# Optimization experiments

Hardware: AMD Instinct MI355X
Metric: run time of the kernel (lower is better)

## Reference

```python
import jax, jax.numpy as jnp
import numpy as np

NUM_HEADS = 32
NUM_KV_HEADS = 8
HEAD_DIM = 128
PAGE_SIZE = 16
NUM_PAGES = 512
PAGES_PER_SEQ = 256  # 4096 cached tokens
Q_LEN = 1024
SCALE = 0.08838834764831845  # 1/sqrt(HEAD_DIM)


def setup_inputs() -> dict:
    key = jax.random.key(0)
    k1, k2, k3, k4, k5 = jax.random.split(key, 5)
    q = jax.random.normal(k1, (Q_LEN, NUM_HEADS * HEAD_DIM), dtype=jnp.float32)
    k = jax.random.normal(k2, (Q_LEN, NUM_KV_HEADS * HEAD_DIM), dtype=jnp.float32)
    v = jax.random.normal(k3, (Q_LEN, NUM_KV_HEADS * HEAD_DIM), dtype=jnp.float32)
    # paged KV cache: [num_pages, 2 (k/v), num_kv_heads, page_size, head_dim]
    kv_cache = jax.random.normal(
        k4, (NUM_PAGES, 2, NUM_KV_HEADS, PAGE_SIZE, HEAD_DIM), dtype=jnp.float32)
    block_table = jnp.sort(
        jax.random.randint(k5, (PAGES_PER_SEQ,), 0, NUM_PAGES, dtype=jnp.int32))
    return {"q": q, "k": k, "v": v, "kv_cache": kv_cache,
            "block_table": block_table}


def reference(q, k, v, kv_cache, block_table):
    # reshape flat projections into heads
    q = q.reshape(-1, NUM_HEADS, HEAD_DIM)          # [Tq, H, D]
    k = k.reshape(-1, NUM_KV_HEADS, HEAD_DIM)       # [Tq, Hkv, D]
    v = v.reshape(-1, NUM_KV_HEADS, HEAD_DIM)

    # gather paged KV cache into continuous tensors (all pages full)
    pages = kv_cache[block_table]                   # [P, 2, Hkv, ps, D]
    # per-page [Hkv, ps, D] -> [ps, Hkv, D], then concat along token dim
    past = jnp.transpose(pages, (1, 0, 3, 2, 4))    # [2, P, ps, Hkv, D]
    past = past.reshape(2, -1, NUM_KV_HEADS, HEAD_DIM)
    past_k, past_v = past[0], past[1]               # [Tpast, Hkv, D]

    k_full = jnp.concatenate([past_k, k], axis=0)   # [Tkv, Hkv, D]
    v_full = jnp.concatenate([past_v, v], axis=0)

    # GQA: repeat kv heads to match query heads
    heads_per_kv = NUM_HEADS // NUM_KV_HEADS
    k_full = jnp.repeat(k_full, heads_per_kv, axis=1)  # [Tkv, H, D]
    v_full = jnp.repeat(v_full, heads_per_kv, axis=1)

    qh = jnp.transpose(q, (1, 0, 2))                # [H, Tq, D]
    kh = jnp.transpose(k_full, (1, 0, 2))           # [H, Tkv, D]
    vh = jnp.transpose(v_full, (1, 0, 2))

    scores = jnp.einsum('hqd,hkd->hqk', qh, kh) * SCALE  # [H, Tq, Tkv]

    # prefill causal mask exactly as in the source: triu(ones(q_len, kv_len), 1)
    q_len, kv_len = qh.shape[1], kh.shape[1]
    causal = jnp.triu(jnp.ones((q_len, kv_len), dtype=bool), k=1)
    scores = jnp.where(causal[None, :, :], -jnp.inf, scores)

    attn = jax.nn.softmax(scores.astype(jnp.float32), axis=-1).astype(qh.dtype)
    out = jnp.einsum('hqk,hkd->hqd', attn, vh)      # [H, Tq, D]
    out = jnp.transpose(out, (1, 0, 2)).reshape(-1, NUM_HEADS * HEAD_DIM)
    return out
```

## Files before the change

### kernel.cpp

```cpp
#include <hip/hip_runtime.h>
#include <hip/hip_bf16.h>


#define Q_STRIDE 4096
#define SCALE 0.08838834764831845f
#define RESCALE_THR 8.0f
#define KSW_TILE 16384
#define VSW_OFF  (2 * 1024 * 1024)
#define ACC1_OFF (4 * 1024 * 1024)
#define ML0_OFF  (ACC1_OFF + 32768 * 256)
#define ML1_OFF  (ML0_OFF + 32768 * 8)

typedef short short8 __attribute__((ext_vector_type(8)));
typedef float f32x4 __attribute__((ext_vector_type(4)));
typedef unsigned short ushort_t;
typedef unsigned int uint_t;

__device__ __forceinline__ ushort_t f2bf(float f) {
    return __builtin_bit_cast(ushort_t, __float2bfloat16(f));
}
__device__ __forceinline__ uint_t pk2(float a, float b) {
    return (uint_t)f2bf(a) | ((uint_t)f2bf(b) << 16);
}
__device__ __forceinline__ float bf2f(ushort_t u) {
    uint_t x = ((uint_t)u) << 16;
    return __builtin_bit_cast(float, x);
}

__launch_bounds__(256)
__global__ void prep_kv(const float* __restrict__ kvc,
                        const int* __restrict__ bt,
                        char* __restrict__ wsb)
{
    __shared__ float sVt[64 * 128];
    const int blk = blockIdx.x;
    const int hkv = blk >> 4;
    const int jb  = blk & 15;
    const int tid = threadIdx.x;
    char* kout = wsb + (size_t)(hkv * 16 + jb) * KSW_TILE;
    char* vout = wsb + VSW_OFF + (size_t)(hkv * 16 + jb) * KSW_TILE;

#pragma unroll
    for (int i = 0; i < 4; ++i) {
        const int u = tid + i * 256;
        const int t = u >> 4, c = u & 15;
        const int gtok = jb * 64 + t;
        const int page = bt[gtok >> 4];
        const float* src = kvc + (size_t)page * 32768 + (size_t)hkv * 2048
                         + (gtok & 15) * 128 + c * 8;
        float4 a = *(const float4*)src;
        float4 b = *(const float4*)(src + 4);
        uint4 p;
        p.x = pk2(a.x, a.y); p.y = pk2(a.z, a.w);
        p.z = pk2(b.x, b.y); p.w = pk2(b.z, b.w);
        *(uint4*)(kout + t * 256 + ((c * 16) ^ ((t & 7) << 4))) = p;
    }
#pragma unroll
    for (int i = 0; i < 8; ++i) {
        const int u = tid + i * 256;
        const int t = u >> 5, c4 = u & 31;
        const int gtok = jb * 64 + t;
        const int page = bt[gtok >> 4];
        const float* src = kvc + (size_t)page * 32768 + 16384
                         + (size_t)hkv * 2048 + (gtok & 15) * 128 + c4 * 4;
        *(float4*)(sVt + t * 128 + c4 * 4) = *(const float4*)src;
    }
    __syncthreads();
#pragma unroll
    for (int i = 0; i < 4; ++i) {
        const int u = tid + i * 256;
        const int d = u >> 3, ch = u & 7;
        float v[8];
#pragma unroll
        for (int k = 0; k < 8; ++k) v[k] = sVt[(8 * ch + k) * 128 + d];
        uint4 p;
        p.x = pk2(v[0], v[1]); p.y = pk2(v[2], v[3]);
        p.z = pk2(v[4], v[5]); p.w = pk2(v[6], v[7]);
        *(uint4*)(vout + ((d * 128 + 16 * ch) ^ ((d & 7) << 4))) = p;
    }
}

#define GLL16(G, L) __builtin_amdgcn_global_load_lds(                         \
    (const uint_t __attribute__((address_space(1)))*)(G),                     \
    (uint_t __attribute__((address_space(3)))*)(L), 16, 0, 0)

#define STAGE(JB, KB, VB) {                                                   \
    const char* b_ = kvbf + (size_t)(hkv * 16 + (JB)) * KSW_TILE              \
                   + w * 1024 + lane * 16;                                    \
    GLL16(b_,                  (KB) + w * 1024);                              \
    GLL16(b_ + 8192,           (KB) + w * 1024 + 8192);                       \
    GLL16(b_ + VSW_OFF,        (VB) + w * 1024);                              \
    GLL16(b_ + VSW_OFF + 8192, (VB) + w * 1024 + 8192);                       \
}

__launch_bounds__(512)
__global__ void attn_main(const float* __restrict__ q,
                          const char* __restrict__ kvbf,
                          float* __restrict__ out,
                          char* __restrict__ wsb)
{
    __shared__ __align__(16) char sK[2][16384];
    __shared__ __align__(16) char sV[2][16384];
    __shared__ __align__(16) char sP[8][2048];

    const int bid  = blockIdx.x;
    const int half = bid >> 8;
    const int rr   = bid & 255;
    const int g    = rr >> 4;
    const int hp   = rr & 15;
    const int qt   = half ? g : (15 - g);
    const int nt   = qt + 1;
    const int nt0  = (nt + 1) >> 1;
    const int jb0  = half ? nt0 : 0;
    const int jb1  = half ? nt  : nt0;
    const int hkv  = hp >> 1;
    const int tid  = threadIdx.x;
    const int w    = tid >> 6;
    const int lane = tid & 63;
    const int l15  = lane & 15;
    const int lhi  = lane >> 4;
    const int h    = hp * 2 + (w >> 2);
    const int rg   = w & 3;

    short8 qf[4];
    {
        const int qrow = qt * 64 + rg * 16 + l15;
        const float* qp = q + (size_t)qrow * Q_STRIDE + h * 128;
#pragma unroll
        for (int s = 0; s < 4; ++s) {
            const int d0 = s * 32 + lhi * 8;
            float4 a = *(const float4*)(qp + d0);
            float4 b = *(const float4*)(qp + d0 + 4);
            short8 v;
            v[0] = (short)f2bf(a.x * SCALE); v[1] = (short)f2bf(a.y * SCALE);
            v[2] = (short)f2bf(a.z * SCALE); v[3] = (short)f2bf(a.w * SCALE);
            v[4] = (short)f2bf(b.x * SCALE); v[5] = (short)f2bf(b.y * SCALE);
            v[6] = (short)f2bf(b.z * SCALE); v[7] = (short)f2bf(b.w * SCALE);
            qf[s] = v;
        }
    }

    f32x4 acc[8];
#pragma unroll
    for (int n2 = 0; n2 < 8; ++n2) acc[n2] = (f32x4){0.f, 0.f, 0.f, 0.f};
    float m_run[4]  = {-1e30f, -1e30f, -1e30f, -1e30f};
    float l_part[4] = {0.f, 0.f, 0.f, 0.f};

    if (jb0 < jb1) {
        STAGE(jb0, sK[0], sV[0])
    }
    __syncthreads();

    for (int jb = jb0; jb < jb1; ++jb) {
        const int cur = (jb - jb0) & 1;
        char* kbuf = sK[cur];
        char* vbuf = sV[cur];
        const bool pf = (jb + 1 < jb1);
        if (pf) {
            STAGE(jb + 1, sK[cur ^ 1], sV[cur ^ 1])
        }

        f32x4 sacc[4];
#pragma unroll
        for (int n = 0; n < 4; ++n) sacc[n] = (f32x4){0.f, 0.f, 0.f, 0.f};
#pragma unroll
        for (int s = 0; s < 4; ++s) {
#pragma unroll
            for (int n = 0; n < 4; ++n) {
                const int tok = n * 16 + l15;
                const uint_t byte = (uint_t)(tok * 256)
                    + (((uint_t)((s * 32 + lhi * 8) * 2)) ^ ((uint_t)((tok & 7) << 4)));
                short8 kb = *(const short8*)(kbuf + byte);
                sacc[n] = __builtin_amdgcn_mfma_f32_16x16x32_bf16(qf[s], kb, sacc[n], 0, 0, 0);
            }
        }

        const bool diag = (jb == qt);
        if (diag) {
#pragma unroll
            for (int n = 0; n < 4; ++n)
#pragma unroll
                for (int j = 0; j < 4; ++j) {
                    const int tok = jb * 64 + n * 16 + l15;
                    const int qg  = qt * 64 + rg * 16 + lhi * 4 + j;
                    if (tok > qg) sacc[n][j] = -1e30f;
                }
        }
#pragma unroll
        for (int j = 0; j < 4; ++j) {
            float lmax = fmaxf(fmaxf(sacc[0][j], sacc[1][j]),
                               fmaxf(sacc[2][j], sacc[3][j]));
            if (__any(lmax > m_run[j] + RESCALE_THR)) {
                float mt = lmax;
#pragma unroll
                for (int off = 1; off < 16; off <<= 1)
                    mt = fmaxf(mt, __shfl_xor(mt, off));
                const float mn = fmaxf(m_run[j], mt);
                const float alpha = __expf(m_run[j] - mn);
                m_run[j] = mn;
                l_part[j] *= alpha;
#pragma unroll
                for (int n2 = 0; n2 < 8; ++n2) acc[n2][j] *= alpha;
            }
            float ls = 0.f;
#pragma unroll
            for (int n = 0; n < 4; ++n) {
                float p = __expf(sacc[n][j] - m_run[j]);
                sacc[n][j] = p;
                ls += p;
            }
            l_part[j] += ls;
        }

        char* pb = sP[w];
#pragma unroll
        for (int n = 0; n < 4; ++n)
#pragma unroll
            for (int j = 0; j < 4; ++j) {
                const int r = lhi * 4 + j;
                const uint_t byte = (uint_t)(r * 128)
                    + (((uint_t)((n * 16 + l15) * 2)) ^ ((uint_t)((r & 7) << 4)));
                *(ushort_t*)(pb + byte) = f2bf(sacc[n][j]);
            }

#pragma unroll
        for (int s2 = 0; s2 < 2; ++s2) {
            const uint_t pbyte = (uint_t)(l15 * 128)
                + (((uint_t)((s2 * 32 + lhi * 8) * 2)) ^ ((uint_t)((l15 & 7) << 4)));
            short8 pa = *(const short8*)(pb + pbyte);
#pragma unroll
            for (int n2 = 0; n2 < 8; ++n2) {
                const int dim = n2 * 16 + l15;
                const uint_t vbyte = (uint_t)(dim * 128)
                    + (((uint_t)((s2 * 32 + lhi * 8) * 2)) ^ ((uint_t)((dim & 7) << 4)));
                short8 vbf = *(const short8*)(vbuf + vbyte);
                acc[n2] = __builtin_amdgcn_mfma_f32_16x16x32_bf16(pa, vbf, acc[n2], 0, 0, 0);
            }
        }

        if (pf) __syncthreads();
    }

#pragma unroll
    for (int j = 0; j < 4; ++j) {
        float lsum = l_part[j];
#pragma unroll
        for (int off = 1; off < 16; off <<= 1)
            lsum += __shfl_xor(lsum, off);
        const int row64 = rg * 16 + lhi * 4 + j;
        const int qg    = qt * 64 + row64;
        const int idx   = (qt * 32 + h) * 64 + row64;
        if (half == 0) {
            float* dst = out + (size_t)qg * Q_STRIDE + h * 128;
#pragma unroll
            for (int n2 = 0; n2 < 8; ++n2)
                dst[n2 * 16 + l15] = acc[n2][j];
            if (l15 == 0) {
                float* ml = (float*)(wsb + ML0_OFF) + (size_t)idx * 2;
                ml[0] = m_run[j]; ml[1] = lsum;
            }
        } else {
            ushort_t* dst = (ushort_t*)(wsb + ACC1_OFF) + (size_t)idx * 128;
#pragma unroll
            for (int n2 = 0; n2 < 8; ++n2)
                dst[n2 * 16 + l15] = f2bf(acc[n2][j]);
            if (l15 == 0) {
                float* ml = (float*)(wsb + ML1_OFF) + (size_t)idx * 2;
                ml[0] = m_run[j]; ml[1] = lsum;
            }
        }
    }
}

__launch_bounds__(256)
__global__ void attn_combine(float* __restrict__ out, const char* __restrict__ wsb)
{
    const int pid = blockIdx.x;
    const int qt = pid >> 5;
    const int h  = pid & 31;
    const int tid = threadIdx.x;
    const int d4  = (tid & 31) * 4;
    const float* ml0b = (const float*)(wsb + ML0_OFF);
    const float* ml1b = (const float*)(wsb + ML1_OFF);
    const ushort_t* a1b = (const ushort_t*)(wsb + ACC1_OFF);

#pragma unroll
    for (int p = 0; p < 8; ++p) {
        const int r = (tid >> 5) + p * 8;
        const size_t idx = (size_t)pid * 64 + r;
        const float m1 = ml0b[idx * 2], l1 = ml0b[idx * 2 + 1];
        const float m2 = ml1b[idx * 2], l2 = ml1b[idx * 2 + 1];
        const float m  = fmaxf(m1, m2);
        const float a1 = __expf(m1 - m), a2 = __expf(m2 - m);
        const float inv = 1.0f / (l1 * a1 + l2 * a2);
        float* o = out + (size_t)(qt * 64 + r) * Q_STRIDE + h * 128 + d4;
        const ushort_t* y4 = a1b + idx * 128 + d4;
        float4 x = *(const float4*)o;
        x.x = (x.x * a1 + bf2f(y4[0]) * a2) * inv;
        x.y = (x.y * a1 + bf2f(y4[1]) * a2) * inv;
        x.z = (x.z * a1 + bf2f(y4[2]) * a2) * inv;
        x.w = (x.w * a1 + bf2f(y4[3]) * a2) * inv;
        *(float4*)o = x;
    }
}

extern "C" void kernel_launch(void* const* d_in, const int* in_sizes, int n_in,
                              void* d_out, int out_size, void* d_ws, size_t ws_size,
                              hipStream_t stream) {
    const float* q   = (const float*)d_in[0];
    const float* kvc = (const float*)d_in[3];
    const int*   bt  = (const int*)d_in[4];
    float* out = (float*)d_out;
    char*  wsb = (char*)d_ws;
    prep_kv<<<dim3(128), dim3(256), 0, stream>>>(kvc, bt, wsb);
    attn_main<<<dim3(512), dim3(512), 0, stream>>>(q, wsb, out, wsb);
    attn_combine<<<dim3(512), dim3(256), 0, stream>>>(out, wsb);
}
```

Before: 54.37 us.

## Split only long query tiles, read V straight from global, shrink blocks

Blocks now cover one head with 4 waves instead of two heads with 8 waves. Only the longer query tiles (8-15) are split into two halves that need a combine pass; short tiles (0-7) run in a single block and write normalized output directly. V is no longer staged in LDS: each wave loads its V fragments from the pre-converted global buffer into registers, and the V swizzle is dropped to match. This is meant to cut LDS use, raise occupancy and shrink the combine kernel, but it makes V global loads sit on the critical path and doubles K reuse traffic across heads.

```diff
diff --git a/kernel.cpp b/kernel.cpp
--- a/kernel.cpp
+++ b/kernel.cpp
@@ -76,7 +76,7 @@
         uint4 p;
         p.x = pk2(v[0], v[1]); p.y = pk2(v[2], v[3]);
         p.z = pk2(v[4], v[5]); p.w = pk2(v[6], v[7]);
-        *(uint4*)(vout + ((d * 128 + 16 * ch) ^ ((d & 7) << 4))) = p;
+        *(uint4*)(vout + d * 128 + 16 * ch) = p;
     }
 }
 
@@ -84,43 +84,49 @@
     (const uint_t __attribute__((address_space(1)))*)(G),                     \
     (uint_t __attribute__((address_space(3)))*)(L), 16, 0, 0)
 
-#define STAGE(JB, KB, VB) {                                                   \
-    const char* b_ = kvbf + (size_t)(hkv * 16 + (JB)) * KSW_TILE              \
-                   + w * 1024 + lane * 16;                                    \
-    GLL16(b_,                  (KB) + w * 1024);                              \
-    GLL16(b_ + 8192,           (KB) + w * 1024 + 8192);                       \
-    GLL16(b_ + VSW_OFF,        (VB) + w * 1024);                              \
-    GLL16(b_ + VSW_OFF + 8192, (VB) + w * 1024 + 8192);                       \
-}
-
-__launch_bounds__(512)
+#define STAGE_K(JB, KB) {                                                     \
+    const char* ks = kvbf + (size_t)(hkv * 16 + (JB)) * KSW_TILE              \
+                   + w * 4096 + lane * 16;                                    \
+    _Pragma("unroll")                                                         \
+    for (int i = 0; i < 4; ++i)                                               \
+        GLL16(ks + i * 1024, (KB) + w * 4096 + i * 1024);                     \
+}
+
+__launch_bounds__(256, 4)
 __global__ void attn_main(const float* __restrict__ q,
                           const char* __restrict__ kvbf,
                           float* __restrict__ out,
                           char* __restrict__ wsb)
 {
     __shared__ __align__(16) char sK[2][16384];
-    __shared__ __align__(16) char sV[2][16384];
-    __shared__ __align__(16) char sP[8][2048];
-
-    const int bid  = blockIdx.x;
-    const int half = bid >> 8;
-    const int rr   = bid & 255;
-    const int g    = rr >> 4;
-    const int hp   = rr & 15;
-    const int qt   = half ? g : (15 - g);
-    const int nt   = qt + 1;
-    const int nt0  = (nt + 1) >> 1;
-    const int jb0  = half ? nt0 : 0;
-    const int jb1  = half ? nt  : nt0;
-    const int hkv  = hp >> 1;
+    __shared__ __align__(16) char sP[4][2048];
+
+    const int bid = blockIdx.x;
+    int qt, jb0, jb1, h, mode;
+    if (bid < 512) {
+        const int half = bid & 1;
+        const int idx  = bid >> 1;
+        qt  = 15 - (idx >> 5);
+        h   = idx & 31;
+        const int nt  = qt + 1;
+        const int nt0 = (nt + 1) >> 1;
+        jb0 = half ? nt0 : 0;
+        jb1 = half ? nt : nt0;
+        mode = half ? 2 : 1;
+    } else {
+        const int didx = bid - 512;
+        qt  = 7 - (didx >> 5);
+        h   = didx & 31;
+        jb0 = 0; jb1 = qt + 1;
+        mode = 0;
+    }
+    const int hkv = h >> 2;
     const int tid  = threadIdx.x;
     const int w    = tid >> 6;
     const int lane = tid & 63;
     const int l15  = lane & 15;
     const int lhi  = lane >> 4;
-    const int h    = hp * 2 + (w >> 2);
-    const int rg   = w & 3;
+    const int rg   = w;
 
     short8 qf[4];
     {
@@ -146,18 +152,16 @@
     float m_run[4]  = {-1e30f, -1e30f, -1e30f, -1e30f};
     float l_part[4] = {0.f, 0.f, 0.f, 0.f};
 
-    if (jb0 < jb1) {
-        STAGE(jb0, sK[0], sV[0])
-    }
+    STAGE_K(jb0, sK[0])
     __syncthreads();
 
+    char* pb = sP[w];
     for (int jb = jb0; jb < jb1; ++jb) {
         const int cur = (jb - jb0) & 1;
         char* kbuf = sK[cur];
-        char* vbuf = sV[cur];
         const bool pf = (jb + 1 < jb1);
         if (pf) {
-            STAGE(jb + 1, sK[cur ^ 1], sV[cur ^ 1])
+            STAGE_K(jb + 1, sK[cur ^ 1])
         }
 
         f32x4 sacc[4];
@@ -175,6 +179,12 @@
             }
         }
 
+        const char* vt = kvbf + VSW_OFF + (size_t)(hkv * 16 + jb) * KSW_TILE;
+        short8 vb0[8];
+#pragma unroll
+        for (int n2 = 0; n2 < 8; ++n2)
+            vb0[n2] = *(const short8*)(vt + (n2 * 16 + l15) * 128 + lhi * 16);
+
         const bool diag = (jb == qt);
         if (diag) {
 #pragma unroll
@@ -212,7 +222,11 @@
             l_part[j] += ls;
         }
 
-        char* pb = sP[w];
+        short8 vb1[8];
+#pragma unroll
+        for (int n2 = 0; n2 < 8; ++n2)
+            vb1[n2] = *(const short8*)(vt + (n2 * 16 + l15) * 128 + 64 + lhi * 16);
+
 #pragma unroll
         for (int n = 0; n < 4; ++n)
 #pragma unroll
@@ -223,19 +237,19 @@
                 *(ushort_t*)(pb + byte) = f2bf(sacc[n][j]);
             }
 
-#pragma unroll
-        for (int s2 = 0; s2 < 2; ++s2) {
-            const uint_t pbyte = (uint_t)(l15 * 128)
-                + (((uint_t)((s2 * 32 + lhi * 8) * 2)) ^ ((uint_t)((l15 & 7) << 4)));
-            short8 pa = *(const short8*)(pb + pbyte);
-#pragma unroll
-            for (int n2 = 0; n2 < 8; ++n2) {
-                const int dim = n2 * 16 + l15;
-                const uint_t vbyte = (uint_t)(dim * 128)
-                    + (((uint_t)((s2 * 32 + lhi * 8) * 2)) ^ ((uint_t)((dim & 7) << 4)));
-                short8 vbf = *(const short8*)(vbuf + vbyte);
-                acc[n2] = __builtin_amdgcn_mfma_f32_16x16x32_bf16(pa, vbf, acc[n2], 0, 0, 0);
-            }
+        {
+            const uint_t pbyte0 = (uint_t)(l15 * 128)
+                + (((uint_t)((lhi * 8) * 2)) ^ ((uint_t)((l15 & 7) << 4)));
+            short8 pa0 = *(const short8*)(pb + pbyte0);
+#pragma unroll
+            for (int n2 = 0; n2 < 8; ++n2)
+                acc[n2] = __builtin_amdgcn_mfma_f32_16x16x32_bf16(pa0, vb0[n2], acc[n2], 0, 0, 0);
+            const uint_t pbyte1 = (uint_t)(l15 * 128)
+                + (((uint_t)((32 + lhi * 8) * 2)) ^ ((uint_t)((l15 & 7) << 4)));
+            short8 pa1 = *(const short8*)(pb + pbyte1);
+#pragma unroll
+            for (int n2 = 0; n2 < 8; ++n2)
+                acc[n2] = __builtin_amdgcn_mfma_f32_16x16x32_bf16(pa1, vb1[n2], acc[n2], 0, 0, 0);
         }
 
         if (pf) __syncthreads();
@@ -249,24 +263,32 @@
             lsum += __shfl_xor(lsum, off);
         const int row64 = rg * 16 + lhi * 4 + j;
         const int qg    = qt * 64 + row64;
-        const int idx   = (qt * 32 + h) * 64 + row64;
-        if (half == 0) {
+        if (mode == 0) {
+            const float inv = 1.0f / lsum;
             float* dst = out + (size_t)qg * Q_STRIDE + h * 128;
 #pragma unroll
             for (int n2 = 0; n2 < 8; ++n2)
-                dst[n2 * 16 + l15] = acc[n2][j];
-            if (l15 == 0) {
-                float* ml = (float*)(wsb + ML0_OFF) + (size_t)idx * 2;
-                ml[0] = m_run[j]; ml[1] = lsum;
-            }
+                dst[n2 * 16 + l15] = acc[n2][j] * inv;
         } else {
-            ushort_t* dst = (ushort_t*)(wsb + ACC1_OFF) + (size_t)idx * 128;
-#pragma unroll
-            for (int n2 = 0; n2 < 8; ++n2)
-                dst[n2 * 16 + l15] = f2bf(acc[n2][j]);
-            if (l15 == 0) {
-                float* ml = (float*)(wsb + ML1_OFF) + (size_t)idx * 2;
-                ml[0] = m_run[j]; ml[1] = lsum;
+            const int idx = (qt * 32 + h) * 64 + row64;
+            if (mode == 1) {
+                float* dst = out + (size_t)qg * Q_STRIDE + h * 128;
+#pragma unroll
+                for (int n2 = 0; n2 < 8; ++n2)
+                    dst[n2 * 16 + l15] = acc[n2][j];
+                if (l15 == 0) {
+                    float* ml = (float*)(wsb + ML0_OFF) + (size_t)idx * 2;
+                    ml[0] = m_run[j]; ml[1] = lsum;
+                }
+            } else {
+                ushort_t* dst = (ushort_t*)(wsb + ACC1_OFF) + (size_t)idx * 128;
+#pragma unroll
+                for (int n2 = 0; n2 < 8; ++n2)
+                    dst[n2 * 16 + l15] = f2bf(acc[n2][j]);
+                if (l15 == 0) {
+                    float* ml = (float*)(wsb + ML1_OFF) + (size_t)idx * 2;
+                    ml[0] = m_run[j]; ml[1] = lsum;
+                }
             }
         }
     }
@@ -276,7 +298,7 @@
 __global__ void attn_combine(float* __restrict__ out, const char* __restrict__ wsb)
 {
     const int pid = blockIdx.x;
-    const int qt = pid >> 5;
+    const int qt = 8 + (pid >> 5);
     const int h  = pid & 31;
     const int tid = threadIdx.x;
     const int d4  = (tid & 31) * 4;
@@ -287,7 +309,7 @@
 #pragma unroll
     for (int p = 0; p < 8; ++p) {
         const int r = (tid >> 5) + p * 8;
-        const size_t idx = (size_t)pid * 64 + r;
+        const size_t idx = (size_t)(qt * 32 + h) * 64 + r;
         const float m1 = ml0b[idx * 2], l1 = ml0b[idx * 2 + 1];
         const float m2 = ml1b[idx * 2], l2 = ml1b[idx * 2 + 1];
         const float m  = fmaxf(m1, m2);
@@ -313,6 +335,6 @@
     float* out = (float*)d_out;
     char*  wsb = (char*)d_ws;
     prep_kv<<<dim3(128), dim3(256), 0, stream>>>(kvc, bt, wsb);
-    attn_main<<<dim3(512), dim3(512), 0, stream>>>(q, wsb, out, wsb);
-    attn_combine<<<dim3(512), dim3(256), 0, stream>>>(out, wsb);
-}
+    attn_main<<<dim3(768), dim3(256), 0, stream>>>(q, wsb, out, wsb);
+    attn_combine<<<dim3(256), dim3(256), 0, stream>>>(out, wsb);
+}
```

New measurement: 86.76 us. 1.6x slower.
